# Kernel optimization log

Hardware: AMD Instinct MI355X
Metric: run time of the kernel (lower is better)

Reference implementation:

```python
import jax, jax.numpy as jnp
import numpy as np

KT = 1.0

def l2norm(x, eps=1e-12):
    # torch F.normalize(p=2): x / max(||x||, eps)
    n = jnp.sqrt(jnp.sum(x * x, axis=-1, keepdims=True))
    return x / jnp.maximum(n, eps)

def setup_inputs() -> dict:
    key = jax.random.key(0)
    k1, k2, k3 = jax.random.split(key, 3)
    B, T, key_dim, e_dim, n_e = 16, 1024, 256, 256, 512
    key_soft = jax.random.normal(k1, (B, T, key_dim), dtype=jnp.float32)
    # embedding tables init uniform(-1/n_e, 1/n_e) as in the torch module
    keys = jax.random.uniform(k2, (n_e, key_dim), minval=-1.0 / n_e, maxval=1.0 / n_e, dtype=jnp.float32)
    vparams = jax.random.uniform(k3, (n_e, e_dim), minval=-1.0 / n_e, maxval=1.0 / n_e, dtype=jnp.float32)
    return {"key_soft": key_soft, "keys": keys, "vparams": vparams}

def reference(key_soft, keys, vparams):
    # clustering_forward of VQClassifierNN
    ksn = l2norm(key_soft)                                  # [B,T,D]
    keys_norm = l2norm(keys)                                # [n_e,D]
    score_ksh = jnp.einsum('btd,nd->btn', ksn, keys_norm)   # [B,T,n_e]
    score_kss = jnp.einsum('btd,bsd->bts', ksn, ksn)        # [B,T,T]
    # softmax weighting over codebook (score_to_weight)
    w = jax.nn.softmax(score_ksh / KT, axis=-1)
    w = jnp.nan_to_num(w)
    vp_norm = l2norm(vparams)                               # [n_e,E]
    vparams_w = l2norm(jnp.einsum('btn,ne->bte', w, vp_norm))  # [B,T,E]
    score_vpss = jnp.einsum('bte,bse->bts', vparams_w, vparams_w)  # [B,T,T]
    score_vpsh = jnp.einsum('bte,ne->btn', vparams_w, vp_norm)     # [B,T,n_e]
    encoding_indices = jnp.argmax(score_ksh, axis=-1)       # [B,T] int
    vparams_hard = l2norm(vparams[encoding_indices])        # gather + normalize
    # straight-through: grads flow through vparams_w
    vparams_hard = vparams_w + jax.lax.stop_gradient(vparams_hard - vparams_w)
    return (encoding_indices, vparams_w, vparams_hard,
            score_vpss, score_vpsh, score_kss, score_ksh)
```

## Files before the change

kernel.cpp:

```cpp
#include <hip/hip_runtime.h>
#include <hip/hip_bf16.h>

#define BB 16
#define TT 1024
#define DD 256
#define NE 512
#define BT 16384

typedef unsigned short ushort_t;
typedef __attribute__((ext_vector_type(8))) short bf16x8;
typedef __attribute__((ext_vector_type(4))) float f32x4;

#define AS_GLOBAL __attribute__((address_space(1)))
#define AS_SHARED __attribute__((address_space(3)))

static __device__ __forceinline__ ushort_t f2bf(float f) {
    union { float f; unsigned u; } x; x.f = f;
    unsigned r = x.u + 0x7fffu + ((x.u >> 16) & 1u);
    return (ushort_t)(r >> 16);
}

__global__ __launch_bounds__(256) void prep_all(const float* __restrict__ ks,
                                                const float* __restrict__ keys,
                                                const float* __restrict__ vparams,
                                                ushort_t* __restrict__ ksn_bf,
                                                ushort_t* __restrict__ keys_n_bf,
                                                float* __restrict__ vp_n,
                                                ushort_t* __restrict__ vp_n_bf,
                                                ushort_t* __restrict__ vpnT_bf) {
    const int bid = blockIdx.x;
    const int t = threadIdx.x;
    if (bid < 4096) {
        const int row  = bid * 4 + (t >> 6);
        const int lane = t & 63;
        const float4 v = *(const float4*)(ks + (long long)row * DD + lane * 4);
        float ss = v.x * v.x + v.y * v.y + v.z * v.z + v.w * v.w;
        #pragma unroll
        for (int off = 32; off > 0; off >>= 1) ss += __shfl_down(ss, off, 64);
        ss = __shfl(ss, 0, 64);
        const float inv = 1.0f / fmaxf(sqrtf(ss), 1e-12f);
        unsigned long long p =
              (unsigned long long)f2bf(v.x * inv)
            | ((unsigned long long)f2bf(v.y * inv) << 16)
            | ((unsigned long long)f2bf(v.z * inv) << 32)
            | ((unsigned long long)f2bf(v.w * inv) << 48);
        *(unsigned long long*)(ksn_bf + (long long)row * DD + lane * 4) = p;
    } else {
        const int b2 = bid - 4096;
        const bool is_keys = (b2 < NE);
        const int rr = is_keys ? b2 : b2 - NE;
        const float* src = (is_keys ? keys : vparams) + (long long)rr * DD;
        const float v = src[t];
        float ss = v * v;
        #pragma unroll
        for (int off = 32; off > 0; off >>= 1) ss += __shfl_down(ss, off, 64);
        __shared__ float partial[4];
        const int wave = t >> 6, lane = t & 63;
        if (lane == 0) partial[wave] = ss;
        __syncthreads();
        __shared__ float s_inv;
        if (t == 0) {
            float tot = partial[0] + partial[1] + partial[2] + partial[3];
            s_inv = 1.0f / fmaxf(sqrtf(tot), 1e-12f);
        }
        __syncthreads();
        const float r = v * s_inv;
        const ushort_t b = f2bf(r);
        if (is_keys) {
            keys_n_bf[(long long)rr * DD + t] = b;
        } else {
            vp_n[(long long)rr * DD + t] = r;
            vp_n_bf[(long long)rr * DD + t] = b;
            vpnT_bf[(long long)t * NE + rr] = b;
        }
    }
}

__global__ __launch_bounds__(256) void mega_gemm(const ushort_t* __restrict__ Ab,
                                                 const ushort_t* __restrict__ Bb,
                                                 float* __restrict__ Cb,
                                                 const ushort_t* __restrict__ Af,
                                                 const ushort_t* __restrict__ Bf,
                                                 float* __restrict__ Cf) {
    const int bid = blockIdx.x;
    const ushort_t *A, *Bm;
    float* C;
    int bm, bn, ldc;
    if (bid < 1024) {
        const int z = bid >> 6, t6 = bid & 63;
        A  = Ab + (long long)z * TT * DD;
        Bm = Bb + (long long)z * TT * DD;
        C  = Cb + (long long)z * TT * TT;
        bm = (t6 >> 3) * 128; bn = (t6 & 7) * 128; ldc = TT;
    } else {
        const int f = bid - 1024;
        A = Af; Bm = Bf; C = Cf;
        bm = (f >> 2) * 128; bn = (f & 3) * 128; ldc = NE;
    }

    __shared__ ushort_t As[128 * 32];
    __shared__ ushort_t Bs[128 * 32];

    const int tid = threadIdx.x;
    const int wv = tid >> 6;
    const int ln = tid & 63;
    const int srow   = ln >> 2;
    const int schunk = (ln & 3) * 8;
    const int wm = (wv >> 1) * 64;
    const int wn = (wv & 1) * 64;
    const int fr = ln & 15;
    const int fq = (ln >> 4) * 8;

    f32x4 acc[4][4] = {};

    for (int k0 = 0; k0 < DD; k0 += 32) {
        #pragma unroll
        for (int t = 0; t < 2; ++t) {
            const int ra = wv * 32 + t * 16;
            const ushort_t* ga = A + (long long)(bm + ra + srow) * DD + k0 + schunk;
            __builtin_amdgcn_global_load_lds((const AS_GLOBAL void*)ga,
                                             (AS_SHARED void*)&As[ra * 32], 16, 0, 0);
            const ushort_t* gb = Bm + (long long)(bn + ra + srow) * DD + k0 + schunk;
            __builtin_amdgcn_global_load_lds((const AS_GLOBAL void*)gb,
                                             (AS_SHARED void*)&Bs[ra * 32], 16, 0, 0);
        }
        __syncthreads();

        bf16x8 af[4], bfr[4];
        #pragma unroll
        for (int i = 0; i < 4; ++i)
            af[i] = *(const bf16x8*)&As[(wm + i * 16 + fr) * 32 + fq];
        #pragma unroll
        for (int j = 0; j < 4; ++j)
            bfr[j] = *(const bf16x8*)&Bs[(wn + j * 16 + fr) * 32 + fq];
        #pragma unroll
        for (int i = 0; i < 4; ++i)
            #pragma unroll
            for (int j = 0; j < 4; ++j)
                acc[i][j] = __builtin_amdgcn_mfma_f32_16x16x32_bf16(af[i], bfr[j], acc[i][j], 0, 0, 0);
        __syncthreads();
    }

    const int col  = ln & 15;
    const int qrow = (ln >> 4) * 4;
    #pragma unroll
    for (int i = 0; i < 4; ++i)
        #pragma unroll
        for (int j = 0; j < 4; ++j)
            #pragma unroll
            for (int r = 0; r < 4; ++r)
                C[(long long)(bm + wm + i * 16 + qrow + r) * ldc + bn + wn + j * 16 + col] = acc[i][j][r];
}

__global__ __launch_bounds__(256) void softmax_argmax(const float* __restrict__ S,
                                                      const float* __restrict__ ks_raw,
                                                      const float* __restrict__ keys_raw,
                                                      float* __restrict__ idx_out,
                                                      ushort_t* __restrict__ W) {
    const int row = blockIdx.x;
    const long long base = (long long)row * NE;
    const int t = threadIdx.x;
    const float v0 = S[base + t];
    const float v1 = S[base + t + 256];

    float bv = fmaxf(v0, v1);
    #pragma unroll
    for (int off = 32; off > 0; off >>= 1) bv = fmaxf(bv, __shfl_down(bv, off, 64));
    __shared__ float pv[4];
    const int wave = t >> 6, lane = t & 63;
    if (lane == 0) pv[wave] = bv;
    __syncthreads();
    __shared__ float s_max;
    if (t == 0) s_max = fmaxf(fmaxf(pv[0], pv[1]), fmaxf(pv[2], pv[3]));
    __syncthreads();
    const float m = s_max;

    __shared__ int cand[128];
    __shared__ int ncand;
    if (t == 0) ncand = 0;
    __syncthreads();
    const float DELTA = 0.02f;
    if (v0 >= m - DELTA) { int p = atomicAdd(&ncand, 1); if (p < 128) cand[p] = t; }
    if (v1 >= m - DELTA) { int p = atomicAdd(&ncand, 1); if (p < 128) cand[p] = t + 256; }
    __syncthreads();
    const int nc = min(ncand, 128);

    __shared__ double wbv[4];
    __shared__ int    wbi[4];
    {
        double best = -1e300; int besti = 0x7fffffff;
        const float* arow = ks_raw + (long long)row * DD;
        const double a0 = (double)arow[lane];
        const double a1 = (double)arow[lane + 64];
        const double a2 = (double)arow[lane + 128];
        const double a3 = (double)arow[lane + 192];
        for (int k = wave; k < nc; k += 4) {
            const int c = cand[k];
            const float* krow = keys_raw + (long long)c * DD;
            const double b0 = (double)krow[lane];
            const double b1 = (double)krow[lane + 64];
            const double b2 = (double)krow[lane + 128];
            const double b3 = (double)krow[lane + 192];
            double dp = a0 * b0 + a1 * b1 + a2 * b2 + a3 * b3;
            double nb = b0 * b0 + b1 * b1 + b2 * b2 + b3 * b3;
            #pragma unroll
            for (int off = 32; off > 0; off >>= 1) {
                dp += __shfl_down(dp, off, 64);
                nb += __shfl_down(nb, off, 64);
            }
            dp = __shfl(dp, 0, 64);
            nb = __shfl(nb, 0, 64);
            const double d = dp / sqrt(nb);
            if (d > best || (d == best && c < besti)) { best = d; besti = c; }
        }
        if (lane == 0) { wbv[wave] = best; wbi[wave] = besti; }
    }
    __syncthreads();
    if (t == 0) {
        double best = wbv[0]; int besti = wbi[0];
        #pragma unroll
        for (int k = 1; k < 4; ++k)
            if (wbv[k] > best || (wbv[k] == best && wbi[k] < besti)) { best = wbv[k]; besti = wbi[k]; }
        idx_out[row] = (float)besti;
    }

    const float e0 = expf(v0 - m);
    const float e1 = expf(v1 - m);
    float ssum = e0 + e1;
    #pragma unroll
    for (int off = 32; off > 0; off >>= 1) ssum += __shfl_down(ssum, off, 64);
    __shared__ float ps[4];
    if (lane == 0) ps[wave] = ssum;
    __syncthreads();
    __shared__ float s_sum;
    if (t == 0) s_sum = ps[0] + ps[1] + ps[2] + ps[3];
    __syncthreads();
    const float inv = 1.0f / s_sum;
    W[base + t]       = f2bf(e0 * inv);
    W[base + t + 256] = f2bf(e1 * inv);
}

__global__ __launch_bounds__(256) void gemm_vpw_norm(const ushort_t* __restrict__ Aw,
                                                     const ushort_t* __restrict__ BvT,
                                                     const float* __restrict__ idxf,
                                                     const float* __restrict__ vp_n,
                                                     float* __restrict__ vpw,
                                                     ushort_t* __restrict__ vpw_bf,
                                                     float* __restrict__ vph) {
    const int bm = blockIdx.x * 64;

    __shared__ ushort_t As[64 * 32];
    __shared__ ushort_t Bs[256 * 32];

    const int tid = threadIdx.x;
    const int wv = tid >> 6;
    const int ln = tid & 63;
    const int srow   = ln >> 2;
    const int schunk = (ln & 3) * 8;
    const int wn = wv * 64;
    const int fr = ln & 15;
    const int fq = (ln >> 4) * 8;

    f32x4 acc[4][4] = {};

    for (int k0 = 0; k0 < NE; k0 += 32) {
        #pragma unroll
        for (int s = 0; s < 5; ++s) {
            const int g = wv * 5 + s;
            if (g < 4) {
                const ushort_t* ga = Aw + (long long)(bm + g * 16 + srow) * NE + k0 + schunk;
                __builtin_amdgcn_global_load_lds((const AS_GLOBAL void*)ga,
                                                 (AS_SHARED void*)&As[(g * 16) * 32], 16, 0, 0);
            } else {
                const int rb = (g - 4) * 16;
                const ushort_t* gb = BvT + (long long)(rb + srow) * NE + k0 + schunk;
                __builtin_amdgcn_global_load_lds((const AS_GLOBAL void*)gb,
                                                 (AS_SHARED void*)&Bs[rb * 32], 16, 0, 0);
            }
        }
        __syncthreads();

        bf16x8 af[4], bfr[4];
        #pragma unroll
        for (int i = 0; i < 4; ++i)
            af[i] = *(const bf16x8*)&As[(i * 16 + fr) * 32 + fq];
        #pragma unroll
        for (int j = 0; j < 4; ++j)
            bfr[j] = *(const bf16x8*)&Bs[(wn + j * 16 + fr) * 32 + fq];
        #pragma unroll
        for (int i = 0; i < 4; ++i)
            #pragma unroll
            for (int j = 0; j < 4; ++j)
                acc[i][j] = __builtin_amdgcn_mfma_f32_16x16x32_bf16(af[i], bfr[j], acc[i][j], 0, 0, 0);
        __syncthreads();
    }

    __shared__ float sq[64][4];
    __shared__ float inv_s[64];
    __shared__ int   sidx[64];
    const int qrow = (ln >> 4) * 4;
    #pragma unroll
    for (int i = 0; i < 4; ++i) {
        #pragma unroll
        for (int r = 0; r < 4; ++r) {
            float s = 0.0f;
            #pragma unroll
            for (int j = 0; j < 4; ++j) { const float a = acc[i][j][r]; s += a * a; }
            #pragma unroll
            for (int msk = 1; msk < 16; msk <<= 1) s += __shfl_xor(s, msk, 64);
            if ((ln & 15) == 0) sq[i * 16 + qrow + r][wv] = s;
        }
    }
    if (tid < 64) sidx[tid] = (int)idxf[bm + tid];
    __syncthreads();
    if (tid < 64) {
        const float tot = sq[tid][0] + sq[tid][1] + sq[tid][2] + sq[tid][3];
        inv_s[tid] = 1.0f / fmaxf(sqrtf(tot), 1e-12f);
    }
    __syncthreads();

    const int col = ln & 15;
    #pragma unroll
    for (int i = 0; i < 4; ++i)
        #pragma unroll
        for (int r = 0; r < 4; ++r) {
            const int row = i * 16 + qrow + r;
            const float iv = inv_s[row];
            #pragma unroll
            for (int j = 0; j < 4; ++j) {
                const float v = acc[i][j][r] * iv;
                const long long o = (long long)(bm + row) * DD + wn + j * 16 + col;
                vpw[o] = v;
                vpw_bf[o] = f2bf(v);
            }
        }

    for (int k = 0; k < 64; ++k) {
        const int grow = bm + k;
        vph[(long long)grow * DD + tid] = vp_n[(long long)sidx[k] * DD + tid];
    }
}

extern "C" void kernel_launch(void* const* d_in, const int* in_sizes, int n_in,
                              void* d_out, int out_size, void* d_ws, size_t ws_size,
                              hipStream_t stream) {
    const float* key_soft = (const float*)d_in[0];
    const float* keys     = (const float*)d_in[1];
    const float* vparams  = (const float*)d_in[2];
    float* out = (float*)d_out;

    const long long off0 = 0;
    const long long off1 = off0 + BT;
    const long long off2 = off1 + (long long)BT * DD;
    const long long off3 = off2 + (long long)BT * DD;
    const long long off4 = off3 + (long long)BB * TT * TT;
    const long long off5 = off4 + (long long)BT * NE;
    const long long off6 = off5 + (long long)BB * TT * TT;

    float* o_idx  = out + off0;
    float* o_vpw  = out + off1;
    float* o_vph  = out + off2;
    float* o_vpss = out + off3;
    float* o_vpsh = out + off4;
    float* o_kss  = out + off5;
    float* o_ksh  = out + off6;

    float*    vp_n      = (float*)d_ws;
    ushort_t* vp_n_bf   = (ushort_t*)(vp_n + (long long)NE * DD);
    ushort_t* vpnT_bf   = vp_n_bf + (long long)NE * DD;
    ushort_t* vpw_bf    = vpnT_bf + (long long)DD * NE;
    ushort_t* keys_n_bf = vpw_bf + (long long)BT * DD;

    ushort_t* ksn_bf = (ushort_t*)o_vpsh;
    ushort_t* w_bf   = (ushort_t*)(o_vpss + (long long)BT * DD);

    prep_all<<<4096 + 2 * NE, 256, 0, stream>>>(
        key_soft, keys, vparams, ksn_bf, keys_n_bf, vp_n, vp_n_bf, vpnT_bf);

    mega_gemm<<<1536, 256, 0, stream>>>(
        ksn_bf, ksn_bf, o_kss, ksn_bf, keys_n_bf, o_ksh);

    softmax_argmax<<<BT, 256, 0, stream>>>(o_ksh, key_soft, keys, o_idx, w_bf);

    gemm_vpw_norm<<<BT / 64, 256, 0, stream>>>(
        w_bf, vpnT_bf, o_idx, vp_n, o_vpw, vpw_bf, o_vph);

    mega_gemm<<<1536, 256, 0, stream>>>(
        vpw_bf, vpw_bf, o_vpss, vpw_bf, vp_n_bf, o_vpsh);
}
```

Measured before the change: 325.6 us.

## Exploit Gram symmetry, double-buffer GEMM LDS, and use one wave per row in softmax

The batched Gram GEMMs (kss, vpss) now compute only the upper-triangular 128x128 tiles and write each off-diagonal tile twice, once transposed. This cuts the MFMA work and operand loads for those products nearly in half, at the price of scattered float4 transposed stores. Both GEMM kernels gain double-buffered LDS staging so the next k-slice loads while the current one computes. softmax_argmax is reorganised so one wave handles one row with vector loads, xor shuffles and ballot-based candidate enumeration, which removes shared-memory reductions and block barriers.

After: 312.0 us. 1.04x faster.

```diff
diff --git a/kernel.cpp b/kernel.cpp
--- a/kernel.cpp
+++ b/kernel.cpp
@@ -8,6 +8,7 @@
 #define BT 16384
 
 typedef unsigned short ushort_t;
+typedef unsigned long long ull_t;
 typedef __attribute__((ext_vector_type(8))) short bf16x8;
 typedef __attribute__((ext_vector_type(4))) float f32x4;
 
@@ -39,12 +40,12 @@
         for (int off = 32; off > 0; off >>= 1) ss += __shfl_down(ss, off, 64);
         ss = __shfl(ss, 0, 64);
         const float inv = 1.0f / fmaxf(sqrtf(ss), 1e-12f);
-        unsigned long long p =
-              (unsigned long long)f2bf(v.x * inv)
-            | ((unsigned long long)f2bf(v.y * inv) << 16)
-            | ((unsigned long long)f2bf(v.z * inv) << 32)
-            | ((unsigned long long)f2bf(v.w * inv) << 48);
-        *(unsigned long long*)(ksn_bf + (long long)row * DD + lane * 4) = p;
+        ull_t p =
+              (ull_t)f2bf(v.x * inv)
+            | ((ull_t)f2bf(v.y * inv) << 16)
+            | ((ull_t)f2bf(v.z * inv) << 32)
+            | ((ull_t)f2bf(v.w * inv) << 48);
+        *(ull_t*)(ksn_bf + (long long)row * DD + lane * 4) = p;
     } else {
         const int b2 = bid - 4096;
         const bool is_keys = (b2 < NE);
@@ -77,7 +78,6 @@
 }
 
 __global__ __launch_bounds__(256) void mega_gemm(const ushort_t* __restrict__ Ab,
-                                                 const ushort_t* __restrict__ Bb,
                                                  float* __restrict__ Cb,
                                                  const ushort_t* __restrict__ Af,
                                                  const ushort_t* __restrict__ Bf,
@@ -86,20 +86,27 @@
     const ushort_t *A, *Bm;
     float* C;
     int bm, bn, ldc;
-    if (bid < 1024) {
-        const int z = bid >> 6, t6 = bid & 63;
+    bool sym;
+    if (bid < 576) {
+        const int z = bid / 36;
+        int tt = bid - z * 36;
+        int i = 0;
+        while (tt >= 8 - i) { tt -= 8 - i; ++i; }
+        const int j = i + tt;
         A  = Ab + (long long)z * TT * DD;
-        Bm = Bb + (long long)z * TT * DD;
+        Bm = A;
         C  = Cb + (long long)z * TT * TT;
-        bm = (t6 >> 3) * 128; bn = (t6 & 7) * 128; ldc = TT;
+        bm = i * 128; bn = j * 128; ldc = TT;
+        sym = (i != j);
     } else {
-        const int f = bid - 1024;
+        const int f = bid - 576;
         A = Af; Bm = Bf; C = Cf;
         bm = (f >> 2) * 128; bn = (f & 3) * 128; ldc = NE;
-    }
-
-    __shared__ ushort_t As[128 * 32];
-    __shared__ ushort_t Bs[128 * 32];
+        sym = false;
+    }
+
+    __shared__ ushort_t As[2][128 * 32];
+    __shared__ ushort_t Bs[2][128 * 32];
 
     const int tid = threadIdx.x;
     const int wv = tid >> 6;
@@ -113,33 +120,47 @@
 
     f32x4 acc[4][4] = {};
 
-    for (int k0 = 0; k0 < DD; k0 += 32) {
-        #pragma unroll
-        for (int t = 0; t < 2; ++t) {
-            const int ra = wv * 32 + t * 16;
-            const ushort_t* ga = A + (long long)(bm + ra + srow) * DD + k0 + schunk;
-            __builtin_amdgcn_global_load_lds((const AS_GLOBAL void*)ga,
-                                             (AS_SHARED void*)&As[ra * 32], 16, 0, 0);
-            const ushort_t* gb = Bm + (long long)(bn + ra + srow) * DD + k0 + schunk;
-            __builtin_amdgcn_global_load_lds((const AS_GLOBAL void*)gb,
-                                             (AS_SHARED void*)&Bs[ra * 32], 16, 0, 0);
-        }
+#define MG_STAGE(buf, kk)                                                          \
+    {                                                                              \
+        _Pragma("unroll")                                                          \
+        for (int s = 0; s < 2; ++s) {                                              \
+            const int ra = wv * 32 + s * 16;                                       \
+            const ushort_t* ga = A + (long long)(bm + ra + srow) * DD + (kk) + schunk; \
+            __builtin_amdgcn_global_load_lds((const AS_GLOBAL void*)ga,            \
+                (AS_SHARED void*)&As[buf][ra * 32], 16, 0, 0);                     \
+            const ushort_t* gb = Bm + (long long)(bn + ra + srow) * DD + (kk) + schunk; \
+            __builtin_amdgcn_global_load_lds((const AS_GLOBAL void*)gb,            \
+                (AS_SHARED void*)&Bs[buf][ra * 32], 16, 0, 0);                     \
+        }                                                                          \
+    }
+
+#define MG_COMPUTE(buf)                                                            \
+    {                                                                              \
+        bf16x8 af[4], bfr[4];                                                      \
+        _Pragma("unroll")                                                          \
+        for (int i = 0; i < 4; ++i)                                                \
+            af[i] = *(const bf16x8*)&As[buf][(wm + i * 16 + fr) * 32 + fq];        \
+        _Pragma("unroll")                                                          \
+        for (int j = 0; j < 4; ++j)                                                \
+            bfr[j] = *(const bf16x8*)&Bs[buf][(wn + j * 16 + fr) * 32 + fq];       \
+        _Pragma("unroll")                                                          \
+        for (int i = 0; i < 4; ++i)                                                \
+            _Pragma("unroll")                                                      \
+            for (int j = 0; j < 4; ++j)                                            \
+                acc[i][j] = __builtin_amdgcn_mfma_f32_16x16x32_bf16(af[i], bfr[j], acc[i][j], 0, 0, 0); \
+    }
+
+    MG_STAGE(0, 0);
+    __syncthreads();
+    int cur = 0;
+    #pragma unroll
+    for (int k0 = 32; k0 < DD; k0 += 32) {
+        MG_STAGE(cur ^ 1, k0);
+        MG_COMPUTE(cur);
         __syncthreads();
-
-        bf16x8 af[4], bfr[4];
-        #pragma unroll
-        for (int i = 0; i < 4; ++i)
-            af[i] = *(const bf16x8*)&As[(wm + i * 16 + fr) * 32 + fq];
-        #pragma unroll
-        for (int j = 0; j < 4; ++j)
-            bfr[j] = *(const bf16x8*)&Bs[(wn + j * 16 + fr) * 32 + fq];
-        #pragma unroll
-        for (int i = 0; i < 4; ++i)
-            #pragma unroll
-            for (int j = 0; j < 4; ++j)
-                acc[i][j] = __builtin_amdgcn_mfma_f32_16x16x32_bf16(af[i], bfr[j], acc[i][j], 0, 0, 0);
-        __syncthreads();
-    }
+        cur ^= 1;
+    }
+    MG_COMPUTE(cur);
 
     const int col  = ln & 15;
     const int qrow = (ln >> 4) * 4;
@@ -150,6 +171,18 @@
             #pragma unroll
             for (int r = 0; r < 4; ++r)
                 C[(long long)(bm + wm + i * 16 + qrow + r) * ldc + bn + wn + j * 16 + col] = acc[i][j][r];
+
+    if (sym) {
+        #pragma unroll
+        for (int i = 0; i < 4; ++i)
+            #pragma unroll
+            for (int j = 0; j < 4; ++j) {
+                float4 v = make_float4(acc[i][j][0], acc[i][j][1], acc[i][j][2], acc[i][j][3]);
+                *(float4*)&C[(long long)(bn + wn + j * 16 + col) * ldc + bm + wm + i * 16 + qrow] = v;
+            }
+    }
+#undef MG_STAGE
+#undef MG_COMPUTE
 }
 
 __global__ __launch_bounds__(256) void softmax_argmax(const float* __restrict__ S,
@@ -157,87 +190,64 @@
                                                       const float* __restrict__ keys_raw,
                                                       float* __restrict__ idx_out,
                                                       ushort_t* __restrict__ W) {
-    const int row = blockIdx.x;
+    const int row  = blockIdx.x * 4 + (threadIdx.x >> 6);
+    const int lane = threadIdx.x & 63;
     const long long base = (long long)row * NE;
-    const int t = threadIdx.x;
-    const float v0 = S[base + t];
-    const float v1 = S[base + t + 256];
-
-    float bv = fmaxf(v0, v1);
-    #pragma unroll
-    for (int off = 32; off > 0; off >>= 1) bv = fmaxf(bv, __shfl_down(bv, off, 64));
-    __shared__ float pv[4];
-    const int wave = t >> 6, lane = t & 63;
-    if (lane == 0) pv[wave] = bv;
-    __syncthreads();
-    __shared__ float s_max;
-    if (t == 0) s_max = fmaxf(fmaxf(pv[0], pv[1]), fmaxf(pv[2], pv[3]));
-    __syncthreads();
-    const float m = s_max;
-
-    __shared__ int cand[128];
-    __shared__ int ncand;
-    if (t == 0) ncand = 0;
-    __syncthreads();
-    const float DELTA = 0.02f;
-    if (v0 >= m - DELTA) { int p = atomicAdd(&ncand, 1); if (p < 128) cand[p] = t; }
-    if (v1 >= m - DELTA) { int p = atomicAdd(&ncand, 1); if (p < 128) cand[p] = t + 256; }
-    __syncthreads();
-    const int nc = min(ncand, 128);
-
-    __shared__ double wbv[4];
-    __shared__ int    wbi[4];
-    {
-        double best = -1e300; int besti = 0x7fffffff;
-        const float* arow = ks_raw + (long long)row * DD;
-        const double a0 = (double)arow[lane];
-        const double a1 = (double)arow[lane + 64];
-        const double a2 = (double)arow[lane + 128];
-        const double a3 = (double)arow[lane + 192];
-        for (int k = wave; k < nc; k += 4) {
-            const int c = cand[k];
-            const float* krow = keys_raw + (long long)c * DD;
-            const double b0 = (double)krow[lane];
-            const double b1 = (double)krow[lane + 64];
-            const double b2 = (double)krow[lane + 128];
-            const double b3 = (double)krow[lane + 192];
-            double dp = a0 * b0 + a1 * b1 + a2 * b2 + a3 * b3;
-            double nb = b0 * b0 + b1 * b1 + b2 * b2 + b3 * b3;
+
+    const float4 va = *(const float4*)(S + base + lane * 4);
+    const float4 vb = *(const float4*)(S + base + 256 + lane * 4);
+
+    float m8 = fmaxf(fmaxf(fmaxf(va.x, va.y), fmaxf(va.z, va.w)),
+                     fmaxf(fmaxf(vb.x, vb.y), fmaxf(vb.z, vb.w)));
+    #pragma unroll
+    for (int off = 32; off > 0; off >>= 1) m8 = fmaxf(m8, __shfl_xor(m8, off, 64));
+    const float m = m8;
+
+    const float thr = m - 0.02f;
+    unsigned mask = (va.x >= thr ? 1u : 0u) | (va.y >= thr ? 2u : 0u)
+                  | (va.z >= thr ? 4u : 0u) | (va.w >= thr ? 8u : 0u)
+                  | (vb.x >= thr ? 16u : 0u) | (vb.y >= thr ? 32u : 0u)
+                  | (vb.z >= thr ? 64u : 0u) | (vb.w >= thr ? 128u : 0u);
+    ull_t bal = __ballot(mask != 0);
+
+    const float4 af = *(const float4*)(ks_raw + (long long)row * DD + lane * 4);
+    double best = -1e300; int besti = 0x7fffffff;
+    while (bal) {
+        const int src = (int)__builtin_ctzll(bal);
+        bal &= bal - 1;
+        unsigned sm = (unsigned)__shfl((int)mask, src, 64);
+        while (sm) {
+            const int slot = __builtin_ctz(sm);
+            sm &= sm - 1;
+            const int c = (slot < 4) ? (src * 4 + slot) : (256 + src * 4 + slot - 4);
+            const float4 bf4 = *(const float4*)(keys_raw + (long long)c * DD + lane * 4);
+            double dp = (double)af.x * (double)bf4.x + (double)af.y * (double)bf4.y
+                      + (double)af.z * (double)bf4.z + (double)af.w * (double)bf4.w;
+            double nb = (double)bf4.x * (double)bf4.x + (double)bf4.y * (double)bf4.y
+                      + (double)bf4.z * (double)bf4.z + (double)bf4.w * (double)bf4.w;
             #pragma unroll
             for (int off = 32; off > 0; off >>= 1) {
-                dp += __shfl_down(dp, off, 64);
-                nb += __shfl_down(nb, off, 64);
+                dp += __shfl_xor(dp, off, 64);
+                nb += __shfl_xor(nb, off, 64);
             }
-            dp = __shfl(dp, 0, 64);
-            nb = __shfl(nb, 0, 64);
             const double d = dp / sqrt(nb);
             if (d > best || (d == best && c < besti)) { best = d; besti = c; }
         }
-        if (lane == 0) { wbv[wave] = best; wbi[wave] = besti; }
-    }
-    __syncthreads();
-    if (t == 0) {
-        double best = wbv[0]; int besti = wbi[0];
-        #pragma unroll
-        for (int k = 1; k < 4; ++k)
-            if (wbv[k] > best || (wbv[k] == best && wbi[k] < besti)) { best = wbv[k]; besti = wbi[k]; }
-        idx_out[row] = (float)besti;
-    }
-
-    const float e0 = expf(v0 - m);
-    const float e1 = expf(v1 - m);
-    float ssum = e0 + e1;
-    #pragma unroll
-    for (int off = 32; off > 0; off >>= 1) ssum += __shfl_down(ssum, off, 64);
-    __shared__ float ps[4];
-    if (lane == 0) ps[wave] = ssum;
-    __syncthreads();
-    __shared__ float s_sum;
-    if (t == 0) s_sum = ps[0] + ps[1] + ps[2] + ps[3];
-    __syncthreads();
-    const float inv = 1.0f / s_sum;
-    W[base + t]       = f2bf(e0 * inv);
-    W[base + t + 256] = f2bf(e1 * inv);
+    }
+    if (lane == 0) idx_out[row] = (float)besti;
+
+    const float e0 = expf(va.x - m), e1 = expf(va.y - m), e2 = expf(va.z - m), e3 = expf(va.w - m);
+    const float e4 = expf(vb.x - m), e5 = expf(vb.y - m), e6 = expf(vb.z - m), e7 = expf(vb.w - m);
+    float ssum = ((e0 + e1) + (e2 + e3)) + ((e4 + e5) + (e6 + e7));
+    #pragma unroll
+    for (int off = 32; off > 0; off >>= 1) ssum += __shfl_xor(ssum, off, 64);
+    const float inv = 1.0f / ssum;
+    ull_t p0 = (ull_t)f2bf(e0 * inv) | ((ull_t)f2bf(e1 * inv) << 16)
+             | ((ull_t)f2bf(e2 * inv) << 32) | ((ull_t)f2bf(e3 * inv) << 48);
+    ull_t p1 = (ull_t)f2bf(e4 * inv) | ((ull_t)f2bf(e5 * inv) << 16)
+             | ((ull_t)f2bf(e6 * inv) << 32) | ((ull_t)f2bf(e7 * inv) << 48);
+    *(ull_t*)(W + base + lane * 4) = p0;
+    *(ull_t*)(W + base + 256 + lane * 4) = p1;
 }
 
 __global__ __launch_bounds__(256) void gemm_vpw_norm(const ushort_t* __restrict__ Aw,
@@ -249,8 +259,8 @@
                                                      float* __restrict__ vph) {
     const int bm = blockIdx.x * 64;
 
-    __shared__ ushort_t As[64 * 32];
-    __shared__ ushort_t Bs[256 * 32];
+    __shared__ ushort_t As[2][64 * 32];
+    __shared__ ushort_t Bs[2][256 * 32];
 
     const int tid = threadIdx.x;
     const int wv = tid >> 6;
@@ -263,37 +273,50 @@
 
     f32x4 acc[4][4] = {};
 
-    for (int k0 = 0; k0 < NE; k0 += 32) {
-        #pragma unroll
-        for (int s = 0; s < 5; ++s) {
-            const int g = wv * 5 + s;
-            if (g < 4) {
-                const ushort_t* ga = Aw + (long long)(bm + g * 16 + srow) * NE + k0 + schunk;
-                __builtin_amdgcn_global_load_lds((const AS_GLOBAL void*)ga,
-                                                 (AS_SHARED void*)&As[(g * 16) * 32], 16, 0, 0);
-            } else {
-                const int rb = (g - 4) * 16;
-                const ushort_t* gb = BvT + (long long)(rb + srow) * NE + k0 + schunk;
-                __builtin_amdgcn_global_load_lds((const AS_GLOBAL void*)gb,
-                                                 (AS_SHARED void*)&Bs[rb * 32], 16, 0, 0);
-            }
-        }
+#define VW_STAGE(buf, kk)                                                          \
+    {                                                                              \
+        _Pragma("unroll")                                                          \
+        for (int s = 0; s < 5; ++s) {                                              \
+            const int g = wv * 5 + s;                                              \
+            if (g < 4) {                                                           \
+                const ushort_t* ga = Aw + (long long)(bm + g * 16 + srow) * NE + (kk) + schunk; \
+                __builtin_amdgcn_global_load_lds((const AS_GLOBAL void*)ga,        \
+                    (AS_SHARED void*)&As[buf][(g * 16) * 32], 16, 0, 0);           \
+            } else {                                                               \
+                const int rb = (g - 4) * 16;                                       \
+                const ushort_t* gb = BvT + (long long)(rb + srow) * NE + (kk) + schunk; \
+                __builtin_amdgcn_global_load_lds((const AS_GLOBAL void*)gb,        \
+                    (AS_SHARED void*)&Bs[buf][rb * 32], 16, 0, 0);                 \
+            }                                                                      \
+        }                                                                          \
+    }
+
+#define VW_COMPUTE(buf)                                                            \
+    {                                                                              \
+        bf16x8 af[4], bfr[4];                                                      \
+        _Pragma("unroll")                                                          \
+        for (int i = 0; i < 4; ++i)                                                \
+            af[i] = *(const bf16x8*)&As[buf][(i * 16 + fr) * 32 + fq];             \
+        _Pragma("unroll")                                                          \
+        for (int j = 0; j < 4; ++j)                                                \
+            bfr[j] = *(const bf16x8*)&Bs[buf][(wn + j * 16 + fr) * 32 + fq];       \
+        _Pragma("unroll")                                                          \
+        for (int i = 0; i < 4; ++i)                                                \
+            _Pragma("unroll")                                                      \
+            for (int j = 0; j < 4; ++j)                                            \
+                acc[i][j] = __builtin_amdgcn_mfma_f32_16x16x32_bf16(af[i], bfr[j], acc[i][j], 0, 0, 0); \
+    }
+
+    VW_STAGE(0, 0);
+    __syncthreads();
+    int cur = 0;
+    for (int k0 = 32; k0 < NE; k0 += 32) {
+        VW_STAGE(cur ^ 1, k0);
+        VW_COMPUTE(cur);
         __syncthreads();
-
-        bf16x8 af[4], bfr[4];
-        #pragma unroll
-        for (int i = 0; i < 4; ++i)
-            af[i] = *(const bf16x8*)&As[(i * 16 + fr) * 32 + fq];
-        #pragma unroll
-        for (int j = 0; j < 4; ++j)
-            bfr[j] = *(const bf16x8*)&Bs[(wn + j * 16 + fr) * 32 + fq];
-        #pragma unroll
-        for (int i = 0; i < 4; ++i)
-            #pragma unroll
-            for (int j = 0; j < 4; ++j)
-                acc[i][j] = __builtin_amdgcn_mfma_f32_16x16x32_bf16(af[i], bfr[j], acc[i][j], 0, 0, 0);
-        __syncthreads();
-    }
+        cur ^= 1;
+    }
+    VW_COMPUTE(cur);
 
     __shared__ float sq[64][4];
     __shared__ float inv_s[64];
@@ -339,6 +362,8 @@
         const int grow = bm + k;
         vph[(long long)grow * DD + tid] = vp_n[(long long)sidx[k] * DD + tid];
     }
+#undef VW_STAGE
+#undef VW_COMPUTE
 }
 
 extern "C" void kernel_launch(void* const* d_in, const int* in_sizes, int n_in,
@@ -377,14 +402,14 @@
     prep_all<<<4096 + 2 * NE, 256, 0, stream>>>(
         key_soft, keys, vparams, ksn_bf, keys_n_bf, vp_n, vp_n_bf, vpnT_bf);
 
-    mega_gemm<<<1536, 256, 0, stream>>>(
-        ksn_bf, ksn_bf, o_kss, ksn_bf, keys_n_bf, o_ksh);
-
-    softmax_argmax<<<BT, 256, 0, stream>>>(o_ksh, key_soft, keys, o_idx, w_bf);
+    mega_gemm<<<576 + 512, 256, 0, stream>>>(
+        ksn_bf, o_kss, ksn_bf, keys_n_bf, o_ksh);
+
+    softmax_argmax<<<BT / 4, 256, 0, stream>>>(o_ksh, key_soft, keys, o_idx, w_bf);
 
     gemm_vpw_norm<<<BT / 64, 256, 0, stream>>>(
         w_bf, vpnT_bf, o_idx, vp_n, o_vpw, vpw_bf, o_vph);
 
-    mega_gemm<<<1536, 256, 0, stream>>>(
-        vpw_bf, vpw_bf, o_vpss, vpw_bf, vp_n_bf, o_vpsh);
-}
+    mega_gemm<<<576 + 512, 256, 0, stream>>>(
+        vpw_bf, o_vpss, vpw_bf, vp_n_bf, o_vpsh);
+}
```
